# Performance work log

Hardware: AMD Instinct MI355X
Metric: run time of the kernel (lower is better)

The kernel has to match this reference:

```python
import jax, jax.numpy as jnp
import numpy as np

BS = 1024
IN_DIM = 16 * 16      # final_dim[0]*final_dim[1]
HIDDEN = 3000
ITEM = 3              # item_number
STEPS = 30


def setup_inputs() -> dict:
    key = jax.random.key(0)
    ks = jax.random.split(key, 16)

    def xavier(k, shape):
        fan_in, fan_out = shape[1], shape[0]
        lim = np.sqrt(6.0 / (fan_in + fan_out))
        return jax.random.uniform(k, shape, jnp.float32, -lim, lim)

    return {
        "z": jax.random.normal(ks[0], (BS, 16, 16), jnp.float32),
        # join MLP: in->512->256->3000, ReLU after each
        "W1": xavier(ks[1], (512, IN_DIM)), "b1": jnp.zeros((512,), jnp.float32),
        "W2": xavier(ks[2], (256, 512)),    "b2": jnp.zeros((256,), jnp.float32),
        "W3": xavier(ks[3], (HIDDEN, 256)), "b3": jnp.zeros((HIDDEN,), jnp.float32),
        # GRUCell (torch layout: rows ordered r, z, n)
        "Wih": xavier(ks[4], (3 * HIDDEN, ITEM)),
        "bih": jnp.zeros((3 * HIDDEN,), jnp.float32),
        "Whh": xavier(ks[5], (3 * HIDDEN, HIDDEN)),
        "bhh": jnp.zeros((3 * HIDDEN,), jnp.float32),
        # output readout hidden -> item_number
        "Wo": xavier(ks[6], (ITEM, HIDDEN)), "bo": jnp.zeros((ITEM,), jnp.float32),
    }


def reference(z, W1, b1, W2, b2, W3, b3, Wih, bih, Whh, bhh, Wo, bo):
    bs = z.shape[0]
    zf = z.reshape(bs, -1)                                  # [bs, 256]
    h = jax.nn.relu(zf @ W1.T + b1)
    h = jax.nn.relu(h @ W2.T + b2)
    h = jax.nn.relu(h @ W3.T + b3)                          # [bs, 3000] initial hidden
    x0 = jnp.zeros((bs, ITEM), z.dtype)

    def step(carry, _):
        h, x = carry
        gi = x @ Wih.T + bih                                # [bs, 3H]
        gh = h @ Whh.T + bhh                                # [bs, 3H]
        i_r, i_z, i_n = jnp.split(gi, 3, axis=-1)
        h_r, h_z, h_n = jnp.split(gh, 3, axis=-1)
        r = jax.nn.sigmoid(i_r + h_r)
        u = jax.nn.sigmoid(i_z + h_z)
        n = jnp.tanh(i_n + r * h_n)
        h_new = (1.0 - u) * n + u * h
        x_new = h_new @ Wo.T + bo + x                       # residual waypoint add
        return (h_new, x_new), x_new

    (_, _), wp = jax.lax.scan(step, (h, x0), None, length=STEPS)
    return jnp.transpose(wp, (1, 0, 2))                      # [bs, STEPS, ITEM]
```

## Files before the change

### kernel.cpp

```cpp
#include <hip/hip_runtime.h>
#include <cstdint>
#include <cstddef>

#define HID 3000
#define HP  3072
#define NB  1024
#define BM  128
#define BN  64
#define KT  48
#define BUFSZ 51200
#define PLANE 13312

typedef _Float16 f16;
typedef _Float16 f16x8 __attribute__((ext_vector_type(8)));
typedef float    f32x4 __attribute__((ext_vector_type(4)));

__device__ __forceinline__ float sigf(float v)  { return 1.0f / (1.0f + __expf(-v)); }
__device__ __forceinline__ float tanhf_(float v){ return 2.0f / (1.0f + __expf(-2.0f * v)) - 1.0f; }

__device__ __forceinline__ void gload16(const void* g, void* l) {
    __builtin_amdgcn_global_load_lds((const __attribute__((address_space(1))) void*)g,
                                     (__attribute__((address_space(3))) void*)l, 16, 0, 0);
}

__global__ __launch_bounds__(256) void convert_whh(const float* __restrict__ whh,
                                                   f16* __restrict__ whh16)
{
    const int S32 = 3 * HP * (HP / 32);
    int t = blockIdx.x * 256 + threadIdx.x;
    if (t >= S32) return;
    const int c32 = (t % (HP / 32)) * 32;
    const int rr  = (t / (HP / 32)) % HP;
    const int g   = t / ((HP / 32) * HP);
    f16* dst = whh16 + ((size_t)g * HP + rr) * HP + c32;
    if (rr < HID && c32 + 32 <= HID) {
        const float* src = whh + (size_t)(g * HID + rr) * HID + c32;
#pragma unroll
        for (int u = 0; u < 4; ++u) {
            float4 lo = *reinterpret_cast<const float4*>(src + u * 8);
            float4 hi = *reinterpret_cast<const float4*>(src + u * 8 + 4);
            f16x8 v;
            v[0] = (f16)lo.x; v[1] = (f16)lo.y; v[2] = (f16)lo.z; v[3] = (f16)lo.w;
            v[4] = (f16)hi.x; v[5] = (f16)hi.y; v[6] = (f16)hi.z; v[7] = (f16)hi.w;
            *reinterpret_cast<f16x8*>(dst + u * 8) = v;
        }
    } else {
#pragma unroll
        for (int u = 0; u < 4; ++u) {
            f16x8 v;
#pragma unroll
            for (int k = 0; k < 8; ++k) {
                const int cc = c32 + u * 8 + k;
                v[k] = (rr < HID && cc < HID) ? (f16)whh[(size_t)(g * HID + rr) * HID + cc]
                                              : (f16)0.0f;
            }
            *reinterpret_cast<f16x8*>(dst + u * 8) = v;
        }
    }
}

__global__ __launch_bounds__(256) void convert_w3(const float* __restrict__ w,
                                                  f16* __restrict__ w16)
{
    int t = blockIdx.x * 256 + threadIdx.x;
    if (t >= HP * 32) return;
    int rr = t >> 5, c8 = (t & 31) * 8;
    f16x8 v;
    if (rr < HID) {
        const float* src = w + (size_t)rr * 256 + c8;
        float4 lo = *reinterpret_cast<const float4*>(src);
        float4 hi = *reinterpret_cast<const float4*>(src + 4);
        v[0] = (f16)lo.x; v[1] = (f16)lo.y; v[2] = (f16)lo.z; v[3] = (f16)lo.w;
        v[4] = (f16)hi.x; v[5] = (f16)hi.y; v[6] = (f16)hi.z; v[7] = (f16)hi.w;
    } else {
#pragma unroll
        for (int i = 0; i < 8; ++i) v[i] = (f16)0.0f;
    }
    *reinterpret_cast<f16x8*>(w16 + (size_t)rr * 256 + c8) = v;
}

__global__ __launch_bounds__(256) void mlp_layer(const float* __restrict__ A, int K, int N, int ldo,
                                                 const float* __restrict__ W,
                                                 const float* __restrict__ bias,
                                                 float* __restrict__ outf, f16* __restrict__ outh)
{
    __shared__ float sA[4 * 512];
    const int b0 = blockIdx.x * 4;
    for (int idx = threadIdx.x; idx < 4 * K; idx += 256)
        sA[idx] = A[(size_t)b0 * K + idx];
    __syncthreads();
    for (int n = threadIdx.x; n < ldo; n += 256) {
        float acc[4] = {0.f, 0.f, 0.f, 0.f};
        if (n < N) {
            const float4* wr = reinterpret_cast<const float4*>(W + (size_t)n * K);
            for (int kk = 0; kk < (K >> 2); ++kk) {
                float4 w = wr[kk];
#pragma unroll
                for (int r = 0; r < 4; ++r) {
                    const float* ar = sA + r * K + kk * 4;
                    acc[r] += ar[0] * w.x + ar[1] * w.y + ar[2] * w.z + ar[3] * w.w;
                }
            }
            float bv = bias[n];
#pragma unroll
            for (int r = 0; r < 4; ++r) acc[r] = fmaxf(acc[r] + bv, 0.f);
        }
#pragma unroll
        for (int r = 0; r < 4; ++r) {
            outf[(size_t)(b0 + r) * ldo + n] = acc[r];
            if (outh) outh[(size_t)(b0 + r) * ldo + n] = (f16)acc[r];
        }
    }
}

__global__ __launch_bounds__(256, 2)
void mlp3_mfma(const f16* __restrict__ A, const f16* __restrict__ B,
               const float* __restrict__ bias,
               float* __restrict__ outf, f16* __restrict__ outh)
{
    __shared__ __align__(16) char smem[24576];
    char* sBm = smem + 16384;

    const int tid  = threadIdx.x;
    const int lane = tid & 63;
    const int wid  = tid >> 6;
    const int wm = wid >> 1, wn = wid & 1;
    const int l15 = lane & 15, lhi = lane >> 4;
    const int swz = (lane & 7) << 4;

    const int gm0 = blockIdx.y * BM, gn0 = blockIdx.x * BN;

    const f16* a_srcs[4]; char* a_ldst[4];
#pragma unroll
    for (int i = 0; i < 4; ++i) {
        const int d = (i * 4 + wid) * 64 + lane;
        const int r = d >> 3;
        const int c = (d & 7) ^ (r & 7);
        a_srcs[i] = A + (size_t)(gm0 + r) * 256 + c * 8;
        a_ldst[i] = smem + (i * 4 + wid) * 1024;
    }
    const f16* b_srcs[2]; char* b_ldst[2];
#pragma unroll
    for (int i = 0; i < 2; ++i) {
        const int d = (i * 4 + wid) * 64 + lane;
        const int rr = d >> 3;
        const int c = (d & 7) ^ (rr & 7);
        b_srcs[i] = B + (size_t)(gn0 + rr) * 256 + c * 8;
        b_ldst[i] = sBm + (i * 4 + wid) * 1024;
    }

    f32x4 acc[4][2];
#pragma unroll
    for (int m = 0; m < 4; ++m)
#pragma unroll
        for (int n = 0; n < 2; ++n) acc[m][n] = (f32x4){0.f, 0.f, 0.f, 0.f};

    for (int kt = 0; kt < 4; ++kt) {
        const int kg = kt * 64;
#pragma unroll
        for (int i = 0; i < 4; ++i) gload16(a_srcs[i] + kg, a_ldst[i]);
#pragma unroll
        for (int i = 0; i < 2; ++i) gload16(b_srcs[i] + kg, b_ldst[i]);
        __syncthreads();
#pragma unroll
        for (int kk = 0; kk < 2; ++kk) {
            const int ko = (kk * 64 + lhi * 16) ^ swz;
            f16x8 af[4], bf[2];
#pragma unroll
            for (int m = 0; m < 4; ++m)
                af[m] = *reinterpret_cast<const f16x8*>(smem + (wm * 64 + m * 16 + l15) * 128 + ko);
#pragma unroll
            for (int n = 0; n < 2; ++n)
                bf[n] = *reinterpret_cast<const f16x8*>(sBm + (wn * 32 + n * 16 + l15) * 128 + ko);
#pragma unroll
            for (int m = 0; m < 4; ++m)
#pragma unroll
                for (int n = 0; n < 2; ++n)
                    acc[m][n] = __builtin_amdgcn_mfma_f32_16x16x32_f16(af[m], bf[n], acc[m][n], 0, 0, 0);
        }
        __syncthreads();
    }

#pragma unroll
    for (int m = 0; m < 4; ++m) {
#pragma unroll
        for (int e = 0; e < 4; ++e) {
            const int b = gm0 + wm * 64 + m * 16 + lhi * 4 + e;
#pragma unroll
            for (int n = 0; n < 2; ++n) {
                const int j = gn0 + wn * 32 + n * 16 + l15;
                if (j < HID) {
                    float v = fmaxf(acc[m][n][e] + bias[j], 0.f);
                    outf[(size_t)b * HP + j] = v;
                    outh[(size_t)b * HP + j] = (f16)v;
                }
            }
        }
    }
}

__global__ __launch_bounds__(768, 3)
void gru_step(const f16* __restrict__ h16c, float* __restrict__ hf32,
              const f16* __restrict__ whh16,
              const float* __restrict__ xprev,
              const float* __restrict__ Wih, const float* __restrict__ bih,
              const float* __restrict__ bhh,
              f16* __restrict__ h16n)
{
    __shared__ __align__(16) char smem[159744];

    const int tid  = threadIdx.x;
    const int lane = tid & 63;
    const int wid  = tid >> 6;
    const int wm   = wid & 3;
    const int wn   = wid >> 2;
    const int l15 = lane & 15, lhi = lane >> 4;
    const int swz = (lane & 7) << 4;

    const int id = blockIdx.x;
    const int xcd = id & 7, local = id >> 3;
    const int bn = xcd * 8 + (local >> 2), bm = local & 3;
    const int gm0 = bm * 256, gn0 = bn * 48;

    const f16* srcs[5];
#pragma unroll
    for (int i = 0; i < 4; ++i) {
        const int s = i * 768 + tid;
        if (s < 2048) {
            const int r = s >> 3;
            const int c = (s & 7) ^ (r & 7);
            srcs[i] = h16c + (size_t)(gm0 + r) * HP + c * 8;
        } else {
            const int sb = s - 2048;
            const int rr = sb >> 3;
            const int g = rr / 48, jj = rr - g * 48;
            const int c = (sb & 7) ^ (rr & 7);
            srcs[i] = whh16 + (size_t)g * HP * HP + (size_t)(gn0 + jj) * HP + c * 8;
        }
    }
    {
        const int sb = 1024 + tid;
        const int rr = sb >> 3;
        const int g = rr / 48, jj = rr - g * 48;
        const int c = (sb & 7) ^ (rr & 7);
        srcs[4] = whh16 + (size_t)g * HP * HP + (size_t)(gn0 + jj) * HP + c * 8;
    }

    f32x4 acc[4][3];
#pragma unroll
    for (int m = 0; m < 4; ++m)
#pragma unroll
        for (int n = 0; n < 3; ++n) acc[m][n] = (f32x4){0.f, 0.f, 0.f, 0.f};

    auto STAGE = [&](int kt, char* bufc) {
        const int ko = kt * 64;
#pragma unroll
        for (int i = 0; i < 4; ++i)
            gload16(srcs[i] + ko, bufc + (i * 12 + wid) * 1024);
        if (tid < 128) gload16(srcs[4] + ko, bufc + (48 + wid) * 1024);
    };
    auto COMPUTE = [&](const char* bufc) {
#pragma unroll
        for (int kk = 0; kk < 2; ++kk) {
            const int ko = (kk * 64 + lhi * 16) ^ swz;
            f16x8 af[4], bf[3];
#pragma unroll
            for (int m = 0; m < 4; ++m)
                af[m] = *reinterpret_cast<const f16x8*>(bufc + (wm * 64 + m * 16 + l15) * 128 + ko);
#pragma unroll
            for (int n = 0; n < 3; ++n)
                bf[n] = *reinterpret_cast<const f16x8*>(bufc + 32768 + (wn * 48 + n * 16 + l15) * 128 + ko);
            __builtin_amdgcn_s_setprio(1);
#pragma unroll
            for (int m = 0; m < 4; ++m)
#pragma unroll
                for (int n = 0; n < 3; ++n)
                    acc[m][n] = __builtin_amdgcn_mfma_f32_16x16x32_f16(af[m], bf[n], acc[m][n], 0, 0, 0);
            __builtin_amdgcn_s_setprio(0);
        }
    };

    STAGE(0, smem);
    STAGE(1, smem + BUFSZ);

    int cur = 0;
    for (int t = 0; t < KT; ++t) {
        if (t == KT - 1)      asm volatile("s_waitcnt vmcnt(0)" ::: "memory");
        else if (wid < 2)     asm volatile("s_waitcnt vmcnt(5)" ::: "memory");
        else                  asm volatile("s_waitcnt vmcnt(4)" ::: "memory");
        __builtin_amdgcn_s_barrier();
        __builtin_amdgcn_sched_barrier(0);
        if (t + 2 < KT) {
            int b2 = cur + 2; if (b2 >= 3) b2 -= 3;
            STAGE(t + 2, smem + b2 * BUFSZ);
        }
        COMPUTE(smem + cur * BUFSZ);
        ++cur; if (cur == 3) cur = 0;
    }

    __syncthreads();
    float* planes = reinterpret_cast<float*>(smem);
    {
        float* myplane = planes + wn * PLANE;
#pragma unroll
        for (int m = 0; m < 4; ++m)
#pragma unroll
            for (int n = 0; n < 3; ++n)
#pragma unroll
                for (int e = 0; e < 4; ++e)
                    myplane[(wm * 64 + m * 16 + lhi * 4 + e) * 52 + n * 16 + l15] = acc[m][n][e];
    }
    __syncthreads();

#pragma unroll
    for (int cc = 0; cc < 2; ++cc) {
        const int c = tid + cc * 768;
        const int row = c / 6;
        const int coff = (c - row * 6) * 8;
        const int b = gm0 + row;
        const int jb = gn0 + coff;
        if (jb >= HID) continue;
        const float x0 = xprev[b * 4 + 0], x1 = xprev[b * 4 + 1], x2 = xprev[b * 4 + 2];
        const int pb = row * 52 + coff;
        const int nv = (jb + 8 <= HID) ? 8 : (HID - jb);
        float hn[8];
#pragma unroll
        for (int i = 0; i < 8; ++i) {
            if (i < nv) {
                const int j = jb + i;
                const float g0 = planes[pb + i];
                const float g1 = planes[PLANE + pb + i];
                const float g2 = planes[2 * PLANE + pb + i];
                const float* w0 = Wih + (size_t)j * 3;
                const float* w1 = Wih + (size_t)(HID + j) * 3;
                const float* w2 = Wih + (size_t)(2 * HID + j) * 3;
                const float gi0 = x0 * w0[0] + x1 * w0[1] + x2 * w0[2] + bih[j];
                const float gi1 = x0 * w1[0] + x1 * w1[1] + x2 * w1[2] + bih[HID + j];
                const float gi2 = x0 * w2[0] + x1 * w2[1] + x2 * w2[2] + bih[2 * HID + j];
                const float r = sigf(gi0 + g0 + bhh[j]);
                const float u = sigf(gi1 + g1 + bhh[HID + j]);
                const float nn = tanhf_(gi2 + r * (g2 + bhh[2 * HID + j]));
                const float hp_ = hf32[(size_t)b * HP + j];
                hn[i] = (1.f - u) * nn + u * hp_;
            }
        }
        if (nv == 8) {
            f16x8 hv;
#pragma unroll
            for (int i = 0; i < 8; ++i) hv[i] = (f16)hn[i];
            *reinterpret_cast<f16x8*>(h16n + (size_t)b * HP + jb) = hv;
            float4 f0 = {hn[0], hn[1], hn[2], hn[3]};
            float4 f1 = {hn[4], hn[5], hn[6], hn[7]};
            *reinterpret_cast<float4*>(hf32 + (size_t)b * HP + jb) = f0;
            *reinterpret_cast<float4*>(hf32 + (size_t)b * HP + jb + 4) = f1;
        } else {
            for (int i = 0; i < nv; ++i) {
                hf32[(size_t)b * HP + jb + i] = hn[i];
                h16n[(size_t)b * HP + jb + i] = (f16)hn[i];
            }
        }
    }
}

__global__ __launch_bounds__(256) void x_update(const f16* __restrict__ hn,
                                                const float* __restrict__ Wo,
                                                const float* __restrict__ bo,
                                                const float* __restrict__ xp,
                                                float* __restrict__ xn,
                                                float* __restrict__ out, int s)
{
    const int b = blockIdx.x, tid = threadIdx.x;
    float a0 = 0.f, a1 = 0.f, a2 = 0.f;
    for (int ch = tid; ch < 375; ch += 256) {
        const int k = ch * 8;
        f16x8 h8 = *reinterpret_cast<const f16x8*>(hn + (size_t)b * HP + k);
#pragma unroll
        for (int i = 0; i < 8; ++i) {
            float hv = (float)h8[i];
            a0 += hv * Wo[k + i];
            a1 += hv * Wo[HID + k + i];
            a2 += hv * Wo[2 * HID + k + i];
        }
    }
#pragma unroll
    for (int off = 32; off; off >>= 1) {
        a0 += __shfl_down(a0, off);
        a1 += __shfl_down(a1, off);
        a2 += __shfl_down(a2, off);
    }
    __shared__ float red[3][4];
    const int lane = tid & 63, w = tid >> 6;
    if (lane == 0) { red[0][w] = a0; red[1][w] = a1; red[2][w] = a2; }
    __syncthreads();
    if (tid < 3) {
        float sres = red[tid][0] + red[tid][1] + red[tid][2] + red[tid][3];
        float xv = sres + bo[tid] + xp[b * 4 + tid];
        xn[b * 4 + tid] = xv;
        out[((size_t)b * 30 + s) * 3 + tid] = xv;
    }
}

extern "C" void kernel_launch(void* const* d_in, const int* in_sizes, int n_in,
                              void* d_out, int out_size, void* d_ws, size_t ws_size,
                              hipStream_t stream)
{
    (void)in_sizes; (void)n_in; (void)out_size; (void)ws_size;
    const float* z   = (const float*)d_in[0];
    const float* W1  = (const float*)d_in[1];
    const float* b1  = (const float*)d_in[2];
    const float* W2  = (const float*)d_in[3];
    const float* b2  = (const float*)d_in[4];
    const float* W3  = (const float*)d_in[5];
    const float* b3  = (const float*)d_in[6];
    const float* Wih = (const float*)d_in[7];
    const float* bih = (const float*)d_in[8];
    const float* Whh = (const float*)d_in[9];
    const float* bhh = (const float*)d_in[10];
    const float* Wo  = (const float*)d_in[11];
    const float* bo  = (const float*)d_in[12];
    float* out = (float*)d_out;

    char* ws = (char*)d_ws;
    size_t off = 0;
    f16* whh16 = (f16*)(ws + off); off += (size_t)3 * HP * HP * 2;
    f16* h16[2];
    h16[0] = (f16*)(ws + off); off += (size_t)NB * HP * 2;
    h16[1] = (f16*)(ws + off); off += (size_t)NB * HP * 2;
    float* hf  = (float*)(ws + off); off += (size_t)NB * HP * 4;
    float* h1  = (float*)(ws + off); off += (size_t)NB * 512 * 4;
    float* h2  = (float*)(ws + off); off += (size_t)NB * 256 * 4;
    f16*   h2h = (f16*)(ws + off);   off += (size_t)NB * 256 * 2;
    f16*   w3f16 = (f16*)(ws + off); off += (size_t)HP * 256 * 2;
    float* xb  = (float*)(ws + off); off += (size_t)31 * NB * 4 * 4;

    hipMemsetAsync(h16[0], 0, (size_t)2 * NB * HP * 2, stream);
    hipMemsetAsync(xb, 0, (size_t)NB * 4 * 4, stream);

    {
        int s32 = 3 * HP * (HP / 32);
        convert_whh<<<(s32 + 255) / 256, 256, 0, stream>>>(Whh, whh16);
    }
    convert_w3<<<(HP * 32 + 255) / 256, 256, 0, stream>>>(W3, w3f16);

    mlp_layer<<<NB / 4, 256, 0, stream>>>(z,  256, 512, 512, W1, b1, h1, nullptr);
    mlp_layer<<<NB / 4, 256, 0, stream>>>(h1, 512, 256, 256, W2, b2, h2, h2h);
    mlp3_mfma<<<dim3(HP / BN, NB / BM), 256, 0, stream>>>(h2h, w3f16, b3, hf, h16[0]);

    for (int s = 1; s <= 30; ++s) {
        int cur = (s - 1) & 1, nxt = s & 1;
        gru_step<<<256, 768, 0, stream>>>(
            h16[cur], hf, whh16, xb + (size_t)(s - 1) * NB * 4,
            Wih, bih, bhh, h16[nxt]);
        x_update<<<NB, 256, 0, stream>>>(h16[nxt], Wo, bo,
            xb + (size_t)(s - 1) * NB * 4, xb + (size_t)s * NB * 4, out, s - 1);
    }
}
```

Measured before the change: 2.182 ms.

## Retile GRU step to 4-wave blocks holding all three gates in registers

The GRU step kernel moves from 768-thread blocks with a 256x48 output tile to 256-thread blocks with a 128x96 tile. Each wave accumulates the r, z and n gate outputs for the same columns in registers, so the gate epilogue runs directly from accumulators without the shared-memory plane exchange and its extra barriers. The aim is better operand reuse per wave and removal of the LDS round trip. The cost is fewer waves per CU, higher register pressure from 36 accumulator tiles, and scalar uncoalesced epilogue stores in place of vector stores.

```diff
diff --git a/kernel.cpp b/kernel.cpp
--- a/kernel.cpp
+++ b/kernel.cpp
@@ -8,8 +8,7 @@
 #define BM  128
 #define BN  64
 #define KT  48
-#define BUFSZ 51200
-#define PLANE 13312
+#define BUFSZ 53248
 
 typedef _Float16 f16;
 typedef _Float16 f16x8 __attribute__((ext_vector_type(8)));
@@ -199,7 +198,7 @@
     }
 }
 
-__global__ __launch_bounds__(768, 3)
+__global__ __launch_bounds__(256, 1)
 void gru_step(const f16* __restrict__ h16c, float* __restrict__ hf32,
               const f16* __restrict__ whh16,
               const float* __restrict__ xprev,
@@ -212,70 +211,71 @@
     const int tid  = threadIdx.x;
     const int lane = tid & 63;
     const int wid  = tid >> 6;
-    const int wm   = wid & 3;
-    const int wn   = wid >> 2;
+    const int wrow = (wid & 1) * 64;
+    const int wcol = (wid >> 1) * 48;
     const int l15 = lane & 15, lhi = lane >> 4;
     const int swz = (lane & 7) << 4;
 
     const int id = blockIdx.x;
     const int xcd = id & 7, local = id >> 3;
-    const int bn = xcd * 8 + (local >> 2), bm = local & 3;
-    const int gm0 = bm * 256, gn0 = bn * 48;
-
-    const f16* srcs[5];
+    const int bn = xcd * 4 + (local & 3), bm = local >> 2;
+    const int gm0 = bm * 128, gn0 = bn * 96;
+
+    const f16* srcs[13];
 #pragma unroll
     for (int i = 0; i < 4; ++i) {
-        const int s = i * 768 + tid;
-        if (s < 2048) {
-            const int r = s >> 3;
-            const int c = (s & 7) ^ (r & 7);
-            srcs[i] = h16c + (size_t)(gm0 + r) * HP + c * 8;
-        } else {
-            const int sb = s - 2048;
-            const int rr = sb >> 3;
-            const int g = rr / 48, jj = rr - g * 48;
-            const int c = (sb & 7) ^ (rr & 7);
-            srcs[i] = whh16 + (size_t)g * HP * HP + (size_t)(gn0 + jj) * HP + c * 8;
-        }
-    }
-    {
-        const int sb = 1024 + tid;
+        const int s = i * 256 + tid;
+        const int r = s >> 3;
+        const int c = (s & 7) ^ (r & 7);
+        srcs[i] = h16c + (size_t)(gm0 + r) * HP + c * 8;
+    }
+#pragma unroll
+    for (int i = 4; i < 13; ++i) {
+        const int sb = (i - 4) * 256 + tid;
         const int rr = sb >> 3;
-        const int g = rr / 48, jj = rr - g * 48;
+        const int g = rr / 96, jj = rr - g * 96;
         const int c = (sb & 7) ^ (rr & 7);
-        srcs[4] = whh16 + (size_t)g * HP * HP + (size_t)(gn0 + jj) * HP + c * 8;
-    }
-
-    f32x4 acc[4][3];
-#pragma unroll
-    for (int m = 0; m < 4; ++m)
-#pragma unroll
-        for (int n = 0; n < 3; ++n) acc[m][n] = (f32x4){0.f, 0.f, 0.f, 0.f};
-
-    auto STAGE = [&](int kt, char* bufc) {
+        srcs[i] = whh16 + (size_t)g * HP * HP + (size_t)(gn0 + jj) * HP + c * 8;
+    }
+
+    f32x4 acc[3][4][3];
+#pragma unroll
+    for (int g = 0; g < 3; ++g)
+#pragma unroll
+        for (int m = 0; m < 4; ++m)
+#pragma unroll
+            for (int n = 0; n < 3; ++n) acc[g][m][n] = (f32x4){0.f, 0.f, 0.f, 0.f};
+
+    auto STAGE = [&](int kt, char* buf) {
         const int ko = kt * 64;
 #pragma unroll
         for (int i = 0; i < 4; ++i)
-            gload16(srcs[i] + ko, bufc + (i * 12 + wid) * 1024);
-        if (tid < 128) gload16(srcs[4] + ko, bufc + (48 + wid) * 1024);
+            gload16(srcs[i] + ko, buf + i * 4096 + wid * 1024);
+#pragma unroll
+        for (int i = 4; i < 13; ++i)
+            gload16(srcs[i] + ko, buf + 16384 + (i - 4) * 4096 + wid * 1024);
     };
-    auto COMPUTE = [&](const char* bufc) {
+    auto COMPUTE = [&](const char* buf) {
 #pragma unroll
         for (int kk = 0; kk < 2; ++kk) {
             const int ko = (kk * 64 + lhi * 16) ^ swz;
-            f16x8 af[4], bf[3];
+            f16x8 af[4], bf[3][3];
 #pragma unroll
             for (int m = 0; m < 4; ++m)
-                af[m] = *reinterpret_cast<const f16x8*>(bufc + (wm * 64 + m * 16 + l15) * 128 + ko);
-#pragma unroll
-            for (int n = 0; n < 3; ++n)
-                bf[n] = *reinterpret_cast<const f16x8*>(bufc + 32768 + (wn * 48 + n * 16 + l15) * 128 + ko);
+                af[m] = *reinterpret_cast<const f16x8*>(buf + (wrow + m * 16 + l15) * 128 + ko);
+#pragma unroll
+            for (int g = 0; g < 3; ++g)
+#pragma unroll
+                for (int n = 0; n < 3; ++n)
+                    bf[g][n] = *reinterpret_cast<const f16x8*>(buf + 16384 + (g * 96 + wcol + n * 16 + l15) * 128 + ko);
             __builtin_amdgcn_s_setprio(1);
 #pragma unroll
-            for (int m = 0; m < 4; ++m)
-#pragma unroll
-                for (int n = 0; n < 3; ++n)
-                    acc[m][n] = __builtin_amdgcn_mfma_f32_16x16x32_f16(af[m], bf[n], acc[m][n], 0, 0, 0);
+            for (int g = 0; g < 3; ++g)
+#pragma unroll
+                for (int m = 0; m < 4; ++m)
+#pragma unroll
+                    for (int n = 0; n < 3; ++n)
+                        acc[g][m][n] = __builtin_amdgcn_mfma_f32_16x16x32_f16(af[m], bf[g][n], acc[g][m][n], 0, 0, 0);
             __builtin_amdgcn_s_setprio(0);
         }
     };
@@ -285,9 +285,8 @@
 
     int cur = 0;
     for (int t = 0; t < KT; ++t) {
-        if (t == KT - 1)      asm volatile("s_waitcnt vmcnt(0)" ::: "memory");
-        else if (wid < 2)     asm volatile("s_waitcnt vmcnt(5)" ::: "memory");
-        else                  asm volatile("s_waitcnt vmcnt(4)" ::: "memory");
+        if (t == KT - 1) asm volatile("s_waitcnt vmcnt(0)" ::: "memory");
+        else             asm volatile("s_waitcnt vmcnt(13)" ::: "memory");
         __builtin_amdgcn_s_barrier();
         __builtin_amdgcn_sched_barrier(0);
         if (t + 2 < KT) {
@@ -298,65 +297,33 @@
         ++cur; if (cur == 3) cur = 0;
     }
 
-    __syncthreads();
-    float* planes = reinterpret_cast<float*>(smem);
-    {
-        float* myplane = planes + wn * PLANE;
-#pragma unroll
-        for (int m = 0; m < 4; ++m)
-#pragma unroll
-            for (int n = 0; n < 3; ++n)
-#pragma unroll
-                for (int e = 0; e < 4; ++e)
-                    myplane[(wm * 64 + m * 16 + lhi * 4 + e) * 52 + n * 16 + l15] = acc[m][n][e];
-    }
-    __syncthreads();
-
-#pragma unroll
-    for (int cc = 0; cc < 2; ++cc) {
-        const int c = tid + cc * 768;
-        const int row = c / 6;
-        const int coff = (c - row * 6) * 8;
-        const int b = gm0 + row;
-        const int jb = gn0 + coff;
-        if (jb >= HID) continue;
-        const float x0 = xprev[b * 4 + 0], x1 = xprev[b * 4 + 1], x2 = xprev[b * 4 + 2];
-        const int pb = row * 52 + coff;
-        const int nv = (jb + 8 <= HID) ? 8 : (HID - jb);
-        float hn[8];
-#pragma unroll
-        for (int i = 0; i < 8; ++i) {
-            if (i < nv) {
-                const int j = jb + i;
-                const float g0 = planes[pb + i];
-                const float g1 = planes[PLANE + pb + i];
-                const float g2 = planes[2 * PLANE + pb + i];
-                const float* w0 = Wih + (size_t)j * 3;
-                const float* w1 = Wih + (size_t)(HID + j) * 3;
-                const float* w2 = Wih + (size_t)(2 * HID + j) * 3;
-                const float gi0 = x0 * w0[0] + x1 * w0[1] + x2 * w0[2] + bih[j];
-                const float gi1 = x0 * w1[0] + x1 * w1[1] + x2 * w1[2] + bih[HID + j];
-                const float gi2 = x0 * w2[0] + x1 * w2[1] + x2 * w2[2] + bih[2 * HID + j];
-                const float r = sigf(gi0 + g0 + bhh[j]);
-                const float u = sigf(gi1 + g1 + bhh[HID + j]);
-                const float nn = tanhf_(gi2 + r * (g2 + bhh[2 * HID + j]));
-                const float hp_ = hf32[(size_t)b * HP + j];
-                hn[i] = (1.f - u) * nn + u * hp_;
-            }
-        }
-        if (nv == 8) {
-            f16x8 hv;
-#pragma unroll
-            for (int i = 0; i < 8; ++i) hv[i] = (f16)hn[i];
-            *reinterpret_cast<f16x8*>(h16n + (size_t)b * HP + jb) = hv;
-            float4 f0 = {hn[0], hn[1], hn[2], hn[3]};
-            float4 f1 = {hn[4], hn[5], hn[6], hn[7]};
-            *reinterpret_cast<float4*>(hf32 + (size_t)b * HP + jb) = f0;
-            *reinterpret_cast<float4*>(hf32 + (size_t)b * HP + jb + 4) = f1;
-        } else {
-            for (int i = 0; i < nv; ++i) {
-                hf32[(size_t)b * HP + jb + i] = hn[i];
-                h16n[(size_t)b * HP + jb + i] = (f16)hn[i];
+#pragma unroll
+    for (int m = 0; m < 4; ++m) {
+#pragma unroll
+        for (int e = 0; e < 4; ++e) {
+            const int b = gm0 + wrow + m * 16 + lhi * 4 + e;
+            const float x0 = xprev[b * 4 + 0], x1 = xprev[b * 4 + 1], x2 = xprev[b * 4 + 2];
+#pragma unroll
+            for (int n = 0; n < 3; ++n) {
+                const int j = gn0 + wcol + n * 16 + l15;
+                if (j < HID) {
+                    const float g0 = acc[0][m][n][e];
+                    const float g1 = acc[1][m][n][e];
+                    const float g2 = acc[2][m][n][e];
+                    const float* w0 = Wih + (size_t)j * 3;
+                    const float* w1 = Wih + (size_t)(HID + j) * 3;
+                    const float* w2 = Wih + (size_t)(2 * HID + j) * 3;
+                    const float gi0 = x0 * w0[0] + x1 * w0[1] + x2 * w0[2] + bih[j];
+                    const float gi1 = x0 * w1[0] + x1 * w1[1] + x2 * w1[2] + bih[HID + j];
+                    const float gi2 = x0 * w2[0] + x1 * w2[1] + x2 * w2[2] + bih[2 * HID + j];
+                    const float r = sigf(gi0 + g0 + bhh[j]);
+                    const float u = sigf(gi1 + g1 + bhh[HID + j]);
+                    const float nn = tanhf_(gi2 + r * (g2 + bhh[2 * HID + j]));
+                    const float hp_ = hf32[(size_t)b * HP + j];
+                    const float hn = (1.f - u) * nn + u * hp_;
+                    hf32[(size_t)b * HP + j] = hn;
+                    h16n[(size_t)b * HP + j] = (f16)hn;
+                }
             }
         }
     }
@@ -448,7 +415,7 @@
 
     for (int s = 1; s <= 30; ++s) {
         int cur = (s - 1) & 1, nxt = s & 1;
-        gru_step<<<256, 768, 0, stream>>>(
+        gru_step<<<256, 256, 0, stream>>>(
             h16[cur], hf, whh16, xb + (size_t)(s - 1) * NB * 4,
             Wih, bih, bhh, h16[nxt]);
         x_update<<<NB, 256, 0, stream>>>(h16[nxt], Wo, bo,
```

Result: slower. 2.636 ms (+20.8%).
